# Kernel tuning notes

Hardware: AMD Instinct MI355X
Metric: run time of the kernel (lower is better)

## Reference

```python
import jax, jax.numpy as jnp
import numpy as np

# ---- static config ----
B, D, H, W, C = 4, 8, 56, 56, 192
Md, Mh, Mw = 2, 7, 7
Sd, Sh, Sw = 1, 3, 3
NH = 6
HD = C // NH
SCALE = HD ** -0.5
N = Md * Mh * Mw  # 98
NW = (D // Md) * (H // Mh) * (W // Mw)  # 256 windows per batch element


def _rel_pos_index():
    coords = np.stack(np.meshgrid(np.arange(Md), np.arange(Mh), np.arange(Mw), indexing='ij'))
    cf = coords.reshape(3, -1)
    rc = (cf[:, :, None] - cf[:, None, :]).transpose(1, 2, 0)
    rc[..., 0] += Md - 1
    rc[..., 1] += Mh - 1
    rc[..., 2] += Mw - 1
    rc[..., 0] *= (2 * Mh - 1) * (2 * Mw - 1)
    rc[..., 1] *= 2 * Mw - 1
    return rc.sum(-1)  # (N, N) int

REL_IDX = jnp.asarray(_rel_pos_index())


def _build_attn_mask():
    img = np.zeros((D, H, W), dtype=np.float32)
    cnt = 0
    for ds in (slice(0, -Md), slice(-Md, -Sd), slice(-Sd, None)):
        for hs in (slice(0, -Mh), slice(-Mh, -Sh), slice(-Sh, None)):
            for ws in (slice(0, -Mw), slice(-Mw, -Sw), slice(-Sw, None)):
                img[ds, hs, ws] = cnt
                cnt += 1
    mw = img.reshape(D // Md, Md, H // Mh, Mh, W // Mw, Mw)
    mw = mw.transpose(0, 2, 4, 1, 3, 5).reshape(-1, N)  # (NW, N)
    am = mw[:, None, :] - mw[:, :, None]
    return np.where(am != 0, -100.0, 0.0).astype(np.float32)  # (NW, N, N)


def window_partition(x):  # (B, D, H, W, C) -> (B*NW, N, C)
    x = x.reshape(B, D // Md, Md, H // Mh, Mh, W // Mw, Mw, C)
    return x.transpose(0, 1, 3, 5, 2, 4, 6, 7).reshape(-1, N, C)


def window_reverse(w):  # (B*NW, N, C) -> (B, D, H, W, C)
    x = w.reshape(B, D // Md, H // Mh, W // Mw, Md, Mh, Mw, C)
    return x.transpose(0, 1, 4, 2, 5, 3, 6, 7).reshape(B, D, H, W, C)


def layer_norm(x, g, b, eps=1e-5):
    mu = x.mean(-1, keepdims=True)
    var = ((x - mu) ** 2).mean(-1, keepdims=True)
    return (x - mu) * jax.lax.rsqrt(var + eps) * g + b


def setup_inputs() -> dict:
    key = jax.random.key(0)
    ks = jax.random.split(key, 6)
    return {
        'x': jax.random.normal(ks[0], (B, D * H * W, C), jnp.float32),
        'attn_mask': jnp.asarray(_build_attn_mask()),
        'norm1_g': jnp.ones((C,), jnp.float32),
        'norm1_b': jnp.zeros((C,), jnp.float32),
        'qkv_w': jax.random.normal(ks[1], (3 * C, C), jnp.float32) * 0.02,
        'qkv_b': jnp.zeros((3 * C,), jnp.float32),
        'rel_bias': jax.random.normal(ks[2], ((2 * Md - 1) * (2 * Mh - 1) * (2 * Mw - 1), NH), jnp.float32) * 0.02,
        'proj_w': jax.random.normal(ks[3], (C, C), jnp.float32) * 0.02,
        'proj_b': jnp.zeros((C,), jnp.float32),
        'fc1_w': jax.random.normal(ks[4], (C, C), jnp.float32) * 0.02,
        'fc1_b': jnp.zeros((C,), jnp.float32),
    }


def reference(x, attn_mask, norm1_g, norm1_b, qkv_w, qkv_b, rel_bias, proj_w, proj_b, fc1_w, fc1_b):
    shortcut = x
    h = layer_norm(x, norm1_g, norm1_b).reshape(B, D, H, W, C)
    # cyclic shift (dims divisible by window -> no padding needed)
    h = jnp.roll(h, shift=(-Sd, -Sh, -Sw), axis=(1, 2, 3))
    xw = window_partition(h)  # (B*NW, N, C)
    B_ = xw.shape[0]
    qkv = (xw @ qkv_w.T + qkv_b).reshape(B_, N, 3, NH, HD).transpose(2, 0, 3, 1, 4)
    q, k, v = qkv[0], qkv[1], qkv[2]  # (B_, NH, N, HD)
    attn = jnp.einsum('bhnd,bhmd->bhnm', q * SCALE, k)
    bias = rel_bias[REL_IDX.reshape(-1)].reshape(N, N, NH).transpose(2, 0, 1)  # (NH, N, N)
    attn = attn + bias[None]
    # additive shift mask per window
    attn = attn.reshape(B, NW, NH, N, N) + attn_mask[None, :, None]
    attn = jax.nn.softmax(attn.reshape(B_, NH, N, N), axis=-1)
    out = jnp.einsum('bhnm,bhmd->bhnd', attn, v).transpose(0, 2, 1, 3).reshape(B_, N, C)
    out = out @ proj_w.T + proj_b
    h = window_reverse(out)
    h = jnp.roll(h, shift=(Sd, Sh, Sw), axis=(1, 2, 3)).reshape(B, D * H * W, C)
    h = jax.nn.gelu(h @ fc1_w.T + fc1_b, approximate=False)
    return shortcut + h
```

## Files before the change

kernel.cpp:

```cpp
#include <hip/hip_runtime.h>
#include <cstdint>
#include <cstddef>

typedef __bf16 bf16_t;
typedef __bf16 bf16x8 __attribute__((ext_vector_type(8)));
typedef float  f32x4  __attribute__((ext_vector_type(4)));

#define DHW   25088
#define SCALE 0.17677669529663687f

__device__ inline f32x4 mfma16(bf16x8 a, bf16x8 b, f32x4 c) {
  return __builtin_amdgcn_mfma_f32_16x16x32_bf16(a, b, c, 0, 0, 0);
}

__device__ inline size_t wrow_to_grow(int orow) {
  int win = orow / 98, tok = orow % 98;
  int b = win >> 8, wr = win & 255;
  int bd = wr >> 6, bh = (wr >> 3) & 7, bwi = wr & 7;
  int md = tok / 49, mh = (tok / 7) % 7, mw = tok % 7;
  int d = (bd * 2 + md + 1) & 7;
  int h = bh * 7 + mh + 3; if (h >= 56) h -= 56;
  int w = bwi * 7 + mw + 3; if (w >= 56) w -= 56;
  return (size_t)b * DHW + (size_t)((d * 56 + h) * 56 + w);
}

__global__ __launch_bounds__(256) void prep_kernel(
    const float* __restrict__ qkv_w, const float* __restrict__ proj_w,
    const float* __restrict__ fc1_w,
    bf16_t* __restrict__ wq, bf16_t* __restrict__ wp, bf16_t* __restrict__ wf)
{
  int idx = blockIdx.x * 256 + threadIdx.x;
  if (idx < 110592) { wq[idx] = (bf16_t)qkv_w[idx]; return; }
  idx -= 110592;
  if (idx < 36864) { wp[idx] = (bf16_t)proj_w[idx]; return; }
  idx -= 36864;
  if (idx < 36864) { wf[idx] = (bf16_t)fc1_w[idx]; }
}

__global__ __launch_bounds__(256) void prep_bm_kernel(
    const float* __restrict__ rel_bias, const float* __restrict__ mask,
    bf16_t* __restrict__ bmr)
{
  int idx = blockIdx.x * 256 + threadIdx.x;
  int e    = idx & 31;
  int lane = (idx >> 5) & 63;
  int t2   = idx >> 11;
  int mt   = t2 % 7;
  int wh   = t2 / 7;
  int type = wh / 6, h = wh - type * 6;
  int winb = ((type & 4) ? 3 : 0) * 64 + ((type & 2) ? 7 : 0) * 8 + ((type & 1) ? 7 : 0);
  int g = lane >> 4, li = lane & 15;
  int nt2 = e >> 2, v = e & 3;
  int row = mt * 16 + g * 4 + v;
  int col = nt2 * 16 + li;
  float val = -1e30f;
  if (row < 98 && col < 98 && nt2 < 7) {
    int di = row / 49 - col / 49 + 1;
    int hi = (row / 7) % 7 - (col / 7) % 7 + 6;
    int wi = row % 7 - col % 7 + 6;
    int rid = di * 169 + hi * 13 + wi;
    val = mask[winb * 9604 + row * 98 + col] + rel_bias[rid * 6 + h];
  }
  bmr[idx] = (bf16_t)val;
}

__global__ __launch_bounds__(256, 3) void lnqkv_kernel(
    const float* __restrict__ x, const float* __restrict__ gw,
    const float* __restrict__ bw_, const bf16_t* __restrict__ wq,
    const float* __restrict__ qkv_b, bf16_t* __restrict__ qkv)
{
  __shared__ __align__(16) bf16_t As[64][200];
  __shared__ __align__(16) bf16_t Bs[64][200];
  __shared__ float gws[192], bws[192], bias[576];
  int tid = threadIdx.x;
  int row0 = blockIdx.x * 64;
  if (tid < 192) { gws[tid] = gw[tid]; bws[tid] = bw_[tid]; }
  for (int c = tid; c < 576; c += 256) bias[c] = qkv_b[c];

  {
    int r = tid >> 2, part = tid & 3;
    size_t grow = wrow_to_grow(row0 + r);
    const float* xr = x + grow * 192 + part * 48;
    float v[48];
    #pragma unroll
    for (int i = 0; i < 12; i++) *(float4*)&v[i * 4] = *(const float4*)(xr + i * 4);
    float s = 0.f, sq = 0.f;
    #pragma unroll
    for (int i = 0; i < 48; i++) { s += v[i]; sq += v[i] * v[i]; }
    s += __shfl_xor(s, 1, 64); sq += __shfl_xor(sq, 1, 64);
    s += __shfl_xor(s, 2, 64); sq += __shfl_xor(sq, 2, 64);
    float mu = s * (1.0f / 192.0f);
    float var = sq * (1.0f / 192.0f) - mu * mu;
    float rstd = rsqrtf(var + 1e-5f);
    __syncthreads();
    bf16_t nb[48];
    #pragma unroll
    for (int i = 0; i < 48; i++) {
      int c = part * 48 + i;
      nb[i] = (bf16_t)((v[i] - mu) * rstd * gws[c] + bws[c]);
    }
    #pragma unroll
    for (int j = 0; j < 6; j++)
      *(bf16x8*)&As[r][part * 48 + j * 8] = *(bf16x8*)&nb[j * 8];
  }
  __syncthreads();

  int wid = tid >> 6, lane = tid & 63;
  int wm = wid >> 1, wn = wid & 1;
  int g = lane >> 4, li = lane & 15;
  bf16x8 afr[2][6];
  #pragma unroll
  for (int ks = 0; ks < 6; ks++) {
    afr[0][ks] = *(const bf16x8*)&As[wm * 32 + li][ks * 32 + g * 8];
    afr[1][ks] = *(const bf16x8*)&As[wm * 32 + 16 + li][ks * 32 + g * 8];
  }

  uint4 st[6];
  #pragma unroll
  for (int i = 0; i < 6; i++) {
    int c = tid + 256 * i; int rr = c / 24, ck = c % 24;
    st[i] = *(const uint4*)(wq + (size_t)rr * 192 + ck * 8);
  }
  for (int nt = 0; nt < 9; nt++) {
    __syncthreads();
    #pragma unroll
    for (int i = 0; i < 6; i++) {
      int c = tid + 256 * i; int rr = c / 24, ck = c % 24;
      *(uint4*)&Bs[rr][ck * 8] = st[i];
    }
    __syncthreads();
    if (nt < 8) {
      #pragma unroll
      for (int i = 0; i < 6; i++) {
        int c = tid + 256 * i; int rr = c / 24, ck = c % 24;
        st[i] = *(const uint4*)(wq + (size_t)(nt + 1) * 12288 + (size_t)rr * 192 + ck * 8);
      }
    }
    f32x4 acc[2][2] = {};
    #pragma unroll
    for (int ks = 0; ks < 6; ks++) {
      int ko = ks * 32 + g * 8;
      bf16x8 b0 = *(const bf16x8*)&Bs[wn * 32 + li][ko];
      bf16x8 b1 = *(const bf16x8*)&Bs[wn * 32 + 16 + li][ko];
      acc[0][0] = mfma16(afr[0][ks], b0, acc[0][0]);
      acc[0][1] = mfma16(afr[0][ks], b1, acc[0][1]);
      acc[1][0] = mfma16(afr[1][ks], b0, acc[1][0]);
      acc[1][1] = mfma16(afr[1][ks], b1, acc[1][1]);
    }
    #pragma unroll
    for (int mi = 0; mi < 2; mi++)
    #pragma unroll
    for (int ni = 0; ni < 2; ni++)
    #pragma unroll
    for (int v = 0; v < 4; v++) {
      int row = row0 + wm * 32 + mi * 16 + g * 4 + v;
      int col = nt * 64 + wn * 32 + ni * 16 + li;
      qkv[(size_t)row * 576 + col] = (bf16_t)(acc[mi][ni][v] + bias[col]);
    }
  }
}

__global__ __launch_bounds__(448, 6) void attn_kernel(
    const bf16_t* __restrict__ qkv, const bf16_t* __restrict__ bmr,
    bf16_t* __restrict__ ao)
{
  __shared__ __align__(16) bf16_t U[15232];
  __shared__ __align__(16) bf16_t Vt[32][136];
  int bid = blockIdx.x;
  int h = bid % 6, win = bid / 6;
  int winb = win & 255;
  int type = (((winb >> 6) == 3) ? 4 : 0) | ((((winb >> 3) & 7) == 7) ? 2 : 0)
           | (((winb & 7) == 7) ? 1 : 0);
  int tid = threadIdx.x;
  int wid = tid >> 6, lane = tid & 63;
  int mt = wid, g = lane >> 4, li = lane & 15;

  const bf16_t* bmp = bmr + ((((size_t)(type * 6 + h)) * 7 + mt) * 64 + lane) * 32;
  bf16x8 bm0 = *(const bf16x8*)(bmp);
  bf16x8 bm1 = *(const bf16x8*)(bmp + 8);
  bf16x8 bm2 = *(const bf16x8*)(bmp + 16);
  bf16x8 bm3 = *(const bf16x8*)(bmp + 24);

  const bf16_t* base = qkv + (size_t)win * 98 * 576 + h * 32;
  #define QS(r, c) U[(r) * 40 + (c)]
  #define KS(r, c) U[4480 + (r) * 40 + (c)]
  #define PS(r, c) U[(r) * 136 + (c)]
  for (int c = tid; c < 784; c += 448) {
    int cc = c < 392 ? c : c - 392;
    int tok = cc >> 2, part = cc & 3;
    uint4 u = *(const uint4*)(base + (c < 392 ? 0 : 192) + tok * 576 + part * 8);
    if (c < 392) *(uint4*)&QS(tok, part * 8) = u;
    else         *(uint4*)&KS(tok, part * 8) = u;
  }
  if (tid < 112) {
    uint4 z = {0, 0, 0, 0};
    int a = tid >> 6;
    int r = 98 + ((tid & 63) >> 2), part = tid & 3;
    if (r < 112) {
      if (a == 0) *(uint4*)&QS(r, part * 8) = z;
      else        *(uint4*)&KS(r, part * 8) = z;
    }
  }
  if (tid < 392) {
    int tok = tid >> 2, part = tid & 3;
    bf16x8 u = *(const bf16x8*)(base + 384 + tok * 576 + part * 8);
    #pragma unroll
    for (int j = 0; j < 8; j++) Vt[part * 8 + j][tok] = u[j];
  }
  for (int e2 = tid; e2 < 960; e2 += 448) {
    int r = e2 / 30, ci = 98 + e2 % 30;
    Vt[r][ci] = (bf16_t)0.0f;
  }
  __syncthreads();

  bf16x8 af = *(const bf16x8*)&QS(mt * 16 + li, g * 8);
  float logit[7][4];
  #pragma unroll
  for (int nt2 = 0; nt2 < 7; nt2++) {
    bf16x8 bfr = *(const bf16x8*)&KS(nt2 * 16 + li, g * 8);
    f32x4 z = {};
    f32x4 S = mfma16(af, bfr, z);
    #pragma unroll
    for (int v = 0; v < 4; v++) {
      int e = nt2 * 4 + v;
      float bmv = (e < 8) ? (float)bm0[e] : (e < 16) ? (float)bm1[e - 8]
                : (e < 24) ? (float)bm2[e - 16] : (float)bm3[e - 24];
      logit[nt2][v] = S[v] * SCALE + bmv;
    }
  }
  __syncthreads();

  #pragma unroll
  for (int v = 0; v < 4; v++) {
    float mx = logit[0][v];
    #pragma unroll
    for (int nt2 = 1; nt2 < 7; nt2++) mx = fmaxf(mx, logit[nt2][v]);
    #pragma unroll
    for (int off = 1; off < 16; off <<= 1) mx = fmaxf(mx, __shfl_xor(mx, off, 64));
    float se = 0.f;
    #pragma unroll
    for (int nt2 = 0; nt2 < 7; nt2++) {
      float p = __expf(logit[nt2][v] - mx);
      logit[nt2][v] = p; se += p;
    }
    #pragma unroll
    for (int off = 1; off < 16; off <<= 1) se += __shfl_xor(se, off, 64);
    float inv = 1.0f / se;
    int row = mt * 16 + g * 4 + v;
    #pragma unroll
    for (int nt2 = 0; nt2 < 7; nt2++)
      PS(row, nt2 * 16 + li) = (bf16_t)(logit[nt2][v] * inv);
    PS(row, 112 + li) = (bf16_t)0.0f;
  }
  f32x4 o0 = {}, o1 = {};
  #pragma unroll
  for (int ks = 0; ks < 4; ks++) {
    int ko = ks * 32 + g * 8;
    bf16x8 pf = *(const bf16x8*)&PS(mt * 16 + li, ko);
    bf16x8 v0 = *(const bf16x8*)&Vt[li][ko];
    bf16x8 v1 = *(const bf16x8*)&Vt[16 + li][ko];
    o0 = mfma16(pf, v0, o0);
    o1 = mfma16(pf, v1, o1);
  }
  bf16_t* aout = ao + (size_t)win * 98 * 192 + h * 32;
  #pragma unroll
  for (int v = 0; v < 4; v++) {
    int row = mt * 16 + g * 4 + v;
    if (row < 98) {
      aout[(size_t)row * 192 + li]      = (bf16_t)o0[v];
      aout[(size_t)row * 192 + 16 + li] = (bf16_t)o1[v];
    }
  }
  #undef QS
  #undef KS
  #undef PS
}

__global__ __launch_bounds__(256, 3) void pf_kernel(
    const bf16_t* __restrict__ ao, const bf16_t* __restrict__ wp,
    const float* __restrict__ proj_b, const bf16_t* __restrict__ wf,
    const float* __restrict__ fc1_b, const float* __restrict__ x,
    float* __restrict__ out)
{
  __shared__ __align__(16) bf16_t As[64][200];
  __shared__ __align__(16) bf16_t Bs[64][200];
  __shared__ float pb[192], fb[192];
  int tid = threadIdx.x;
  int row0 = blockIdx.x * 64;
  if (tid < 192) { pb[tid] = proj_b[tid]; fb[tid] = fc1_b[tid]; }
  #pragma unroll
  for (int i = 0; i < 6; i++) {
    int c = tid + 256 * i; int rr = c / 24, ck = c % 24;
    *(uint4*)&As[rr][ck * 8] = *(const uint4*)(ao + (size_t)(row0 + rr) * 192 + ck * 8);
  }
  __syncthreads();

  int wid = tid >> 6, lane = tid & 63;
  int wm = wid >> 1, wn = wid & 1;
  int g = lane >> 4, li = lane & 15;
  bf16x8 afr[2][6];
  #pragma unroll
  for (int ks = 0; ks < 6; ks++) {
    afr[0][ks] = *(const bf16x8*)&As[wm * 32 + li][ks * 32 + g * 8];
    afr[1][ks] = *(const bf16x8*)&As[wm * 32 + 16 + li][ks * 32 + g * 8];
  }
  __syncthreads();

  uint4 st[6];
  #pragma unroll
  for (int i = 0; i < 6; i++) {
    int c = tid + 256 * i; int rr = c / 24, ck = c % 24;
    st[i] = *(const uint4*)(wp + (size_t)rr * 192 + ck * 8);
  }
  for (int nt = 0; nt < 3; nt++) {
    __syncthreads();
    #pragma unroll
    for (int i = 0; i < 6; i++) {
      int c = tid + 256 * i; int rr = c / 24, ck = c % 24;
      *(uint4*)&Bs[rr][ck * 8] = st[i];
    }
    __syncthreads();
    if (nt < 2) {
      #pragma unroll
      for (int i = 0; i < 6; i++) {
        int c = tid + 256 * i; int rr = c / 24, ck = c % 24;
        st[i] = *(const uint4*)(wp + (size_t)(nt + 1) * 12288 + (size_t)rr * 192 + ck * 8);
      }
    }
    f32x4 acc[2][2] = {};
    #pragma unroll
    for (int ks = 0; ks < 6; ks++) {
      int ko = ks * 32 + g * 8;
      bf16x8 b0 = *(const bf16x8*)&Bs[wn * 32 + li][ko];
      bf16x8 b1 = *(const bf16x8*)&Bs[wn * 32 + 16 + li][ko];
      acc[0][0] = mfma16(afr[0][ks], b0, acc[0][0]);
      acc[0][1] = mfma16(afr[0][ks], b1, acc[0][1]);
      acc[1][0] = mfma16(afr[1][ks], b0, acc[1][0]);
      acc[1][1] = mfma16(afr[1][ks], b1, acc[1][1]);
    }
    #pragma unroll
    for (int mi = 0; mi < 2; mi++)
    #pragma unroll
    for (int ni = 0; ni < 2; ni++)
    #pragma unroll
    for (int v = 0; v < 4; v++) {
      int rloc = wm * 32 + mi * 16 + g * 4 + v;
      int col = nt * 64 + wn * 32 + ni * 16 + li;
      As[rloc][col] = (bf16_t)(acc[mi][ni][v] + pb[col]);
    }
  }
  __syncthreads();

  bf16x8 a2[2][6];
  #pragma unroll
  for (int ks = 0; ks < 6; ks++) {
    a2[0][ks] = *(const bf16x8*)&As[wm * 32 + li][ks * 32 + g * 8];
    a2[1][ks] = *(const bf16x8*)&As[wm * 32 + 16 + li][ks * 32 + g * 8];
  }
  #pragma unroll
  for (int i = 0; i < 6; i++) {
    int c = tid + 256 * i; int rr = c / 24, ck = c % 24;
    st[i] = *(const uint4*)(wf + (size_t)rr * 192 + ck * 8);
  }
  for (int nt = 0; nt < 3; nt++) {
    __syncthreads();
    #pragma unroll
    for (int i = 0; i < 6; i++) {
      int c = tid + 256 * i; int rr = c / 24, ck = c % 24;
      *(uint4*)&Bs[rr][ck * 8] = st[i];
    }
    __syncthreads();
    if (nt < 2) {
      #pragma unroll
      for (int i = 0; i < 6; i++) {
        int c = tid + 256 * i; int rr = c / 24, ck = c % 24;
        st[i] = *(const uint4*)(wf + (size_t)(nt + 1) * 12288 + (size_t)rr * 192 + ck * 8);
      }
    }
    f32x4 acc[2][2] = {};
    #pragma unroll
    for (int ks = 0; ks < 6; ks++) {
      int ko = ks * 32 + g * 8;
      bf16x8 b0 = *(const bf16x8*)&Bs[wn * 32 + li][ko];
      bf16x8 b1 = *(const bf16x8*)&Bs[wn * 32 + 16 + li][ko];
      acc[0][0] = mfma16(a2[0][ks], b0, acc[0][0]);
      acc[0][1] = mfma16(a2[0][ks], b1, acc[0][1]);
      acc[1][0] = mfma16(a2[1][ks], b0, acc[1][0]);
      acc[1][1] = mfma16(a2[1][ks], b1, acc[1][1]);
    }
    #pragma unroll
    for (int mi = 0; mi < 2; mi++)
    #pragma unroll
    for (int v = 0; v < 4; v++) {
      int rloc = wm * 32 + mi * 16 + g * 4 + v;
      size_t grow = wrow_to_grow(row0 + rloc);
      #pragma unroll
      for (int ni = 0; ni < 2; ni++) {
        int col = nt * 64 + wn * 32 + ni * 16 + li;
        float val = acc[mi][ni][v] + fb[col];
        float ge = 0.5f * val * (1.0f + erff(val * 0.70710678118654752f));
        size_t o = grow * 192 + col;
        out[o] = x[o] + ge;
      }
    }
  }
}

extern "C" void kernel_launch(void* const* d_in, const int* in_sizes, int n_in,
                              void* d_out, int out_size, void* d_ws, size_t ws_size,
                              hipStream_t stream) {
  (void)in_sizes; (void)n_in; (void)out_size; (void)ws_size;
  const float* x         = (const float*)d_in[0];
  const float* attn_mask = (const float*)d_in[1];
  const float* n1g       = (const float*)d_in[2];
  const float* n1b       = (const float*)d_in[3];
  const float* qkv_w     = (const float*)d_in[4];
  const float* qkv_b     = (const float*)d_in[5];
  const float* rel_bias  = (const float*)d_in[6];
  const float* proj_w    = (const float*)d_in[7];
  const float* proj_b    = (const float*)d_in[8];
  const float* fc1_w     = (const float*)d_in[9];
  const float* fc1_b     = (const float*)d_in[10];
  float* out = (float*)d_out;

  char* ws = (char*)d_ws;
  size_t off = 0;
  auto alloc = [&](size_t bytes) -> char* {
    char* p = ws + off;
    off += (bytes + 255) & ~(size_t)255;
    return p;
  };
  bf16_t* wq  = (bf16_t*)alloc(110592 * 2);
  bf16_t* wp  = (bf16_t*)alloc(36864 * 2);
  bf16_t* wf  = (bf16_t*)alloc(36864 * 2);
  bf16_t* bmr = (bf16_t*)alloc((size_t)688128 * 2);
  bf16_t* qkv = (bf16_t*)alloc((size_t)100352 * 576 * 2);
  bf16_t* ao  = (bf16_t*)alloc((size_t)100352 * 192 * 2);

  prep_kernel<<<720, 256, 0, stream>>>(qkv_w, proj_w, fc1_w, wq, wp, wf);
  prep_bm_kernel<<<2688, 256, 0, stream>>>(rel_bias, attn_mask, bmr);
  lnqkv_kernel<<<1568, 256, 0, stream>>>(x, n1g, n1b, wq, qkv_b, qkv);
  attn_kernel<<<6144, 448, 0, stream>>>(qkv, bmr, ao);
  pf_kernel<<<1568, 256, 0, stream>>>(ao, wp, proj_b, wf, fc1_b, x, out);
}
```

Before: 430.9 us.

## Fuse LN+QKV, windowed attention, proj and FC1 into one per-window kernel

Replaces the three kernels (LN+QKV GEMM, per-head attention, proj+FC1) with one kernel that handles a whole 98-token window per block across all six heads. Q, K, V and the attention output stay in LDS, so the large bf16 qkv and ao intermediates are never written to or read back from global memory. Q is pre-scaled before being stored. The cost is a 163 KB LDS footprint, which allows only one 7-wave block per CU, plus a serial loop over heads with many barriers. This lower occupancy may limit latency hiding.

```diff
diff --git a/kernel.cpp b/kernel.cpp
--- a/kernel.cpp
+++ b/kernel.cpp
@@ -64,346 +64,334 @@
   bmr[idx] = (bf16_t)val;
 }
 
-__global__ __launch_bounds__(256, 3) void lnqkv_kernel(
+__global__ __launch_bounds__(448, 2) void fused_kernel(
     const float* __restrict__ x, const float* __restrict__ gw,
     const float* __restrict__ bw_, const bf16_t* __restrict__ wq,
-    const float* __restrict__ qkv_b, bf16_t* __restrict__ qkv)
+    const float* __restrict__ qkv_b, const bf16_t* __restrict__ wp,
+    const float* __restrict__ proj_b, const bf16_t* __restrict__ wf,
+    const float* __restrict__ fc1_b, const bf16_t* __restrict__ bmr,
+    float* __restrict__ out)
 {
-  __shared__ __align__(16) bf16_t As[64][200];
-  __shared__ __align__(16) bf16_t Bs[64][200];
-  __shared__ float gws[192], bws[192], bias[576];
-  int tid = threadIdx.x;
-  int row0 = blockIdx.x * 64;
-  if (tid < 192) { gws[tid] = gw[tid]; bws[tid] = bw_[tid]; }
-  for (int c = tid; c < 576; c += 256) bias[c] = qkv_b[c];
-
-  {
-    int r = tid >> 2, part = tid & 3;
-    size_t grow = wrow_to_grow(row0 + r);
-    const float* xr = x + grow * 192 + part * 48;
-    float v[48];
-    #pragma unroll
-    for (int i = 0; i < 12; i++) *(float4*)&v[i * 4] = *(const float4*)(xr + i * 4);
-    float s = 0.f, sq = 0.f;
-    #pragma unroll
-    for (int i = 0; i < 48; i++) { s += v[i]; sq += v[i] * v[i]; }
-    s += __shfl_xor(s, 1, 64); sq += __shfl_xor(sq, 1, 64);
-    s += __shfl_xor(s, 2, 64); sq += __shfl_xor(sq, 2, 64);
-    float mu = s * (1.0f / 192.0f);
-    float var = sq * (1.0f / 192.0f) - mu * mu;
-    float rstd = rsqrtf(var + 1e-5f);
-    __syncthreads();
-    bf16_t nb[48];
-    #pragma unroll
-    for (int i = 0; i < 48; i++) {
-      int c = part * 48 + i;
-      nb[i] = (bf16_t)((v[i] - mu) * rstd * gws[c] + bws[c]);
-    }
-    #pragma unroll
-    for (int j = 0; j < 6; j++)
-      *(bf16x8*)&As[r][part * 48 + j * 8] = *(bf16x8*)&nb[j * 8];
-  }
-  __syncthreads();
-
-  int wid = tid >> 6, lane = tid & 63;
-  int wm = wid >> 1, wn = wid & 1;
-  int g = lane >> 4, li = lane & 15;
-  bf16x8 afr[2][6];
-  #pragma unroll
-  for (int ks = 0; ks < 6; ks++) {
-    afr[0][ks] = *(const bf16x8*)&As[wm * 32 + li][ks * 32 + g * 8];
-    afr[1][ks] = *(const bf16x8*)&As[wm * 32 + 16 + li][ks * 32 + g * 8];
-  }
-
-  uint4 st[6];
-  #pragma unroll
-  for (int i = 0; i < 6; i++) {
-    int c = tid + 256 * i; int rr = c / 24, ck = c % 24;
-    st[i] = *(const uint4*)(wq + (size_t)rr * 192 + ck * 8);
-  }
-  for (int nt = 0; nt < 9; nt++) {
-    __syncthreads();
-    #pragma unroll
-    for (int i = 0; i < 6; i++) {
-      int c = tid + 256 * i; int rr = c / 24, ck = c % 24;
-      *(uint4*)&Bs[rr][ck * 8] = st[i];
-    }
-    __syncthreads();
-    if (nt < 8) {
-      #pragma unroll
-      for (int i = 0; i < 6; i++) {
-        int c = tid + 256 * i; int rr = c / 24, ck = c % 24;
-        st[i] = *(const uint4*)(wq + (size_t)(nt + 1) * 12288 + (size_t)rr * 192 + ck * 8);
-      }
-    }
-    f32x4 acc[2][2] = {};
-    #pragma unroll
-    for (int ks = 0; ks < 6; ks++) {
-      int ko = ks * 32 + g * 8;
-      bf16x8 b0 = *(const bf16x8*)&Bs[wn * 32 + li][ko];
-      bf16x8 b1 = *(const bf16x8*)&Bs[wn * 32 + 16 + li][ko];
-      acc[0][0] = mfma16(afr[0][ks], b0, acc[0][0]);
-      acc[0][1] = mfma16(afr[0][ks], b1, acc[0][1]);
-      acc[1][0] = mfma16(afr[1][ks], b0, acc[1][0]);
-      acc[1][1] = mfma16(afr[1][ks], b1, acc[1][1]);
-    }
-    #pragma unroll
-    for (int mi = 0; mi < 2; mi++)
-    #pragma unroll
-    for (int ni = 0; ni < 2; ni++)
-    #pragma unroll
-    for (int v = 0; v < 4; v++) {
-      int row = row0 + wm * 32 + mi * 16 + g * 4 + v;
-      int col = nt * 64 + wn * 32 + ni * 16 + li;
-      qkv[(size_t)row * 576 + col] = (bf16_t)(acc[mi][ni][v] + bias[col]);
-    }
-  }
-}
-
-__global__ __launch_bounds__(448, 6) void attn_kernel(
-    const bf16_t* __restrict__ qkv, const bf16_t* __restrict__ bmr,
-    bf16_t* __restrict__ ao)
-{
-  __shared__ __align__(16) bf16_t U[15232];
-  __shared__ __align__(16) bf16_t Vt[32][136];
-  int bid = blockIdx.x;
-  int h = bid % 6, win = bid / 6;
+  __shared__ __align__(16) char smem[163392];
+  bf16_t* U  = (bf16_t*)smem;
+  bf16_t* Qs = (bf16_t*)(smem + 30464);
+  bf16_t* Ks = (bf16_t*)(smem + 69664);
+  bf16_t* Vt = (bf16_t*)(smem + 108864);
+  float*  qb = (float*)(smem + 161088);
+  float* gwb = (float*)smem;
+
+  #define BS(r, c)  U[(r) * 200 + (c)]
+  #define PSd(r, c) U[(r) * 136 + (c)]
+  #define QS(r, c)  Qs[(r) * 200 + (c)]
+  #define KS(r, c)  Ks[(r) * 200 + (c)]
+  #define VT(d, t)  Vt[(d) * 136 + (t)]
+
+  int win  = blockIdx.x;
   int winb = win & 255;
   int type = (((winb >> 6) == 3) ? 4 : 0) | ((((winb >> 3) & 7) == 7) ? 2 : 0)
            | (((winb & 7) == 7) ? 1 : 0);
-  int tid = threadIdx.x;
-  int wid = tid >> 6, lane = tid & 63;
-  int mt = wid, g = lane >> 4, li = lane & 15;
-
-  const bf16_t* bmp = bmr + ((((size_t)(type * 6 + h)) * 7 + mt) * 64 + lane) * 32;
-  bf16x8 bm0 = *(const bf16x8*)(bmp);
-  bf16x8 bm1 = *(const bf16x8*)(bmp + 8);
-  bf16x8 bm2 = *(const bf16x8*)(bmp + 16);
-  bf16x8 bm3 = *(const bf16x8*)(bmp + 24);
-
-  const bf16_t* base = qkv + (size_t)win * 98 * 576 + h * 32;
-  #define QS(r, c) U[(r) * 40 + (c)]
-  #define KS(r, c) U[4480 + (r) * 40 + (c)]
-  #define PS(r, c) U[(r) * 136 + (c)]
-  for (int c = tid; c < 784; c += 448) {
-    int cc = c < 392 ? c : c - 392;
-    int tok = cc >> 2, part = cc & 3;
-    uint4 u = *(const uint4*)(base + (c < 392 ? 0 : 192) + tok * 576 + part * 8);
-    if (c < 392) *(uint4*)&QS(tok, part * 8) = u;
-    else         *(uint4*)&KS(tok, part * 8) = u;
-  }
-  if (tid < 112) {
-    uint4 z = {0, 0, 0, 0};
-    int a = tid >> 6;
-    int r = 98 + ((tid & 63) >> 2), part = tid & 3;
-    if (r < 112) {
-      if (a == 0) *(uint4*)&QS(r, part * 8) = z;
-      else        *(uint4*)&KS(r, part * 8) = z;
-    }
-  }
-  if (tid < 392) {
-    int tok = tid >> 2, part = tid & 3;
-    bf16x8 u = *(const bf16x8*)(base + 384 + tok * 576 + part * 8);
-    #pragma unroll
-    for (int j = 0; j < 8; j++) Vt[part * 8 + j][tok] = u[j];
-  }
-  for (int e2 = tid; e2 < 960; e2 += 448) {
-    int r = e2 / 30, ci = 98 + e2 % 30;
-    Vt[r][ci] = (bf16_t)0.0f;
-  }
+  int tid  = threadIdx.x;
+  int wid  = tid >> 6, lane = tid & 63;
+  int g = lane >> 4, li = lane & 15;
+
+  if (tid < 192) { gwb[tid] = gw[tid]; gwb[192 + tid] = bw_[tid]; }
+  for (int c = tid; c < 576; c += 448) qb[c] = qkv_b[c];
+  {
+    uint4 z = {0u, 0u, 0u, 0u};
+    for (int c = tid; c < 768; c += 448) {
+      int d = c >> 2, part = c & 3;
+      *(uint4*)&VT(d, 96 + part * 8) = z;
+    }
+  }
+
+  int r = wid * 16 + li;
+  float v[48];
+  if (r < 98) {
+    size_t growr = wrow_to_grow(win * 98 + r);
+    const float* xr = x + growr * 192 + g * 8;
+    #pragma unroll
+    for (int ks = 0; ks < 6; ks++) {
+      *(float4*)&v[ks * 8]     = *(const float4*)(xr + ks * 32);
+      *(float4*)&v[ks * 8 + 4] = *(const float4*)(xr + ks * 32 + 4);
+    }
+  } else {
+    #pragma unroll
+    for (int i = 0; i < 48; i++) v[i] = 0.f;
+  }
+  float s = 0.f, sq = 0.f;
+  #pragma unroll
+  for (int i = 0; i < 48; i++) { s += v[i]; sq += v[i] * v[i]; }
+  s += __shfl_xor(s, 16, 64); sq += __shfl_xor(sq, 16, 64);
+  s += __shfl_xor(s, 32, 64); sq += __shfl_xor(sq, 32, 64);
+  float mu   = s * (1.0f / 192.0f);
+  float var  = sq * (1.0f / 192.0f) - mu * mu;
+  float rstd = rsqrtf(var + 1e-5f);
   __syncthreads();
-
-  bf16x8 af = *(const bf16x8*)&QS(mt * 16 + li, g * 8);
-  float logit[7][4];
-  #pragma unroll
-  for (int nt2 = 0; nt2 < 7; nt2++) {
-    bf16x8 bfr = *(const bf16x8*)&KS(nt2 * 16 + li, g * 8);
-    f32x4 z = {};
-    f32x4 S = mfma16(af, bfr, z);
-    #pragma unroll
-    for (int v = 0; v < 4; v++) {
-      int e = nt2 * 4 + v;
-      float bmv = (e < 8) ? (float)bm0[e] : (e < 16) ? (float)bm1[e - 8]
-                : (e < 24) ? (float)bm2[e - 16] : (float)bm3[e - 24];
-      logit[nt2][v] = S[v] * SCALE + bmv;
+  bf16x8 afr[6];
+  #pragma unroll
+  for (int ks = 0; ks < 6; ks++) {
+    bf16x8 t;
+    #pragma unroll
+    for (int j = 0; j < 8; j++) {
+      int c = ks * 32 + g * 8 + j;
+      t[j] = (r < 98) ? (bf16_t)((v[ks * 8 + j] - mu) * rstd * gwb[c] + gwb[192 + c])
+                      : (bf16_t)0.0f;
+    }
+    afr[ks] = t;
+  }
+
+  uint4 st[4];
+  #pragma unroll
+  for (int i = 0; i < 4; i++) {
+    int c = tid + 448 * i;
+    if (i < 3 || c < 1536) {
+      int rr = c / 24, ck = c % 24;
+      st[i] = *(const uint4*)(wq + (size_t)rr * 192 + ck * 8);
+    }
+  }
+  for (int nt = 0; nt < 9; nt++) {
+    __syncthreads();
+    #pragma unroll
+    for (int i = 0; i < 4; i++) {
+      int c = tid + 448 * i;
+      if (i < 3 || c < 1536) {
+        int rr = c / 24, ck = c % 24;
+        *(uint4*)&BS(rr, ck * 8) = st[i];
+      }
+    }
+    __syncthreads();
+    if (nt < 8) {
+      #pragma unroll
+      for (int i = 0; i < 4; i++) {
+        int c = tid + 448 * i;
+        if (i < 3 || c < 1536) {
+          int rr = c / 24, ck = c % 24;
+          st[i] = *(const uint4*)(wq + (size_t)(nt + 1) * 12288 + (size_t)rr * 192 + ck * 8);
+        }
+      }
+    }
+    f32x4 acc[4] = {};
+    #pragma unroll
+    for (int ks = 0; ks < 6; ks++) {
+      bf16x8 a = afr[ks];
+      #pragma unroll
+      for (int ni = 0; ni < 4; ni++) {
+        bf16x8 b = *(const bf16x8*)&BS(ni * 16 + li, ks * 32 + g * 8);
+        acc[ni] = mfma16(a, b, acc[ni]);
+      }
+    }
+    #pragma unroll
+    for (int ni = 0; ni < 4; ni++)
+    #pragma unroll
+    for (int vv = 0; vv < 4; vv++) {
+      int row = wid * 16 + g * 4 + vv;
+      if (row < 98) {
+        int col = nt * 64 + ni * 16 + li;
+        float val = acc[ni][vv] + qb[col];
+        if (nt < 3)      QS(row, col)       = (bf16_t)(val * SCALE);
+        else if (nt < 6) KS(row, col - 192) = (bf16_t)val;
+        else             VT(col - 384, row) = (bf16_t)val;
+      }
     }
   }
   __syncthreads();
 
-  #pragma unroll
-  for (int v = 0; v < 4; v++) {
-    float mx = logit[0][v];
-    #pragma unroll
-    for (int nt2 = 1; nt2 < 7; nt2++) mx = fmaxf(mx, logit[nt2][v]);
-    #pragma unroll
-    for (int off = 1; off < 16; off <<= 1) mx = fmaxf(mx, __shfl_xor(mx, off, 64));
-    float se = 0.f;
+  int mt  = wid;
+  int rq  = mt * 16 + li;
+  int rqc = rq < 98 ? rq : 97;
+  for (int h = 0; h < 6; h++) {
+    const bf16_t* bmp = bmr + ((((size_t)(type * 6 + h)) * 7 + mt) * 64 + lane) * 32;
+    bf16x8 bm0 = *(const bf16x8*)(bmp);
+    bf16x8 bm1 = *(const bf16x8*)(bmp + 8);
+    bf16x8 bm2 = *(const bf16x8*)(bmp + 16);
+    bf16x8 bm3 = *(const bf16x8*)(bmp + 24);
+    bf16x8 af = *(const bf16x8*)&QS(rqc, h * 32 + g * 8);
+    float logit[7][4];
     #pragma unroll
     for (int nt2 = 0; nt2 < 7; nt2++) {
-      float p = __expf(logit[nt2][v] - mx);
-      logit[nt2][v] = p; se += p;
-    }
-    #pragma unroll
-    for (int off = 1; off < 16; off <<= 1) se += __shfl_xor(se, off, 64);
-    float inv = 1.0f / se;
-    int row = mt * 16 + g * 4 + v;
-    #pragma unroll
-    for (int nt2 = 0; nt2 < 7; nt2++)
-      PS(row, nt2 * 16 + li) = (bf16_t)(logit[nt2][v] * inv);
-    PS(row, 112 + li) = (bf16_t)0.0f;
-  }
-  f32x4 o0 = {}, o1 = {};
-  #pragma unroll
-  for (int ks = 0; ks < 4; ks++) {
-    int ko = ks * 32 + g * 8;
-    bf16x8 pf = *(const bf16x8*)&PS(mt * 16 + li, ko);
-    bf16x8 v0 = *(const bf16x8*)&Vt[li][ko];
-    bf16x8 v1 = *(const bf16x8*)&Vt[16 + li][ko];
-    o0 = mfma16(pf, v0, o0);
-    o1 = mfma16(pf, v1, o1);
-  }
-  bf16_t* aout = ao + (size_t)win * 98 * 192 + h * 32;
-  #pragma unroll
-  for (int v = 0; v < 4; v++) {
-    int row = mt * 16 + g * 4 + v;
-    if (row < 98) {
-      aout[(size_t)row * 192 + li]      = (bf16_t)o0[v];
-      aout[(size_t)row * 192 + 16 + li] = (bf16_t)o1[v];
-    }
-  }
+      int rk = nt2 * 16 + li;
+      int rkc = rk < 98 ? rk : 97;
+      bf16x8 bfr = *(const bf16x8*)&KS(rkc, h * 32 + g * 8);
+      f32x4 z = {};
+      f32x4 S = mfma16(af, bfr, z);
+      #pragma unroll
+      for (int vv = 0; vv < 4; vv++) {
+        int e = nt2 * 4 + vv;
+        float bmv = (e < 8) ? (float)bm0[e] : (e < 16) ? (float)bm1[e - 8]
+                  : (e < 24) ? (float)bm2[e - 16] : (float)bm3[e - 24];
+        logit[nt2][vv] = S[vv] + bmv;
+      }
+    }
+    #pragma unroll
+    for (int vv = 0; vv < 4; vv++) {
+      float mx = logit[0][vv];
+      #pragma unroll
+      for (int nt2 = 1; nt2 < 7; nt2++) mx = fmaxf(mx, logit[nt2][vv]);
+      #pragma unroll
+      for (int off = 1; off < 16; off <<= 1) mx = fmaxf(mx, __shfl_xor(mx, off, 64));
+      float se = 0.f;
+      #pragma unroll
+      for (int nt2 = 0; nt2 < 7; nt2++) {
+        float p = __expf(logit[nt2][vv] - mx);
+        logit[nt2][vv] = p; se += p;
+      }
+      #pragma unroll
+      for (int off = 1; off < 16; off <<= 1) se += __shfl_xor(se, off, 64);
+      float inv = 1.0f / se;
+      int row = mt * 16 + g * 4 + vv;
+      #pragma unroll
+      for (int nt2 = 0; nt2 < 7; nt2++)
+        PSd(row, nt2 * 16 + li) = (bf16_t)(logit[nt2][vv] * inv);
+      PSd(row, 112 + li) = (bf16_t)0.0f;
+    }
+    f32x4 o0 = {}, o1 = {};
+    #pragma unroll
+    for (int ks = 0; ks < 4; ks++) {
+      int ko = ks * 32 + g * 8;
+      bf16x8 pf = *(const bf16x8*)&PSd(mt * 16 + li, ko);
+      bf16x8 v0 = *(const bf16x8*)&VT(h * 32 + li, ko);
+      bf16x8 v1 = *(const bf16x8*)&VT(h * 32 + 16 + li, ko);
+      o0 = mfma16(pf, v0, o0);
+      o1 = mfma16(pf, v1, o1);
+    }
+    #pragma unroll
+    for (int vv = 0; vv < 4; vv++) {
+      int row = mt * 16 + g * 4 + vv;
+      if (row < 98) {
+        QS(row, h * 32 + li)      = (bf16_t)o0[vv];
+        QS(row, h * 32 + 16 + li) = (bf16_t)o1[vv];
+      }
+    }
+  }
+
+  float* bfb = qb;
+  if (tid < 192) bfb[tid] = proj_b[tid];
+  bf16x8 a2[6];
+  #pragma unroll
+  for (int ks = 0; ks < 6; ks++)
+    a2[ks] = *(const bf16x8*)&QS(rqc, ks * 32 + g * 8);
+  #pragma unroll
+  for (int i = 0; i < 4; i++) {
+    int c = tid + 448 * i;
+    if (i < 3 || c < 1536) {
+      int rr = c / 24, ck = c % 24;
+      st[i] = *(const uint4*)(wp + (size_t)rr * 192 + ck * 8);
+    }
+  }
+  for (int nt = 0; nt < 3; nt++) {
+    __syncthreads();
+    #pragma unroll
+    for (int i = 0; i < 4; i++) {
+      int c = tid + 448 * i;
+      if (i < 3 || c < 1536) {
+        int rr = c / 24, ck = c % 24;
+        *(uint4*)&BS(rr, ck * 8) = st[i];
+      }
+    }
+    __syncthreads();
+    if (nt < 2) {
+      #pragma unroll
+      for (int i = 0; i < 4; i++) {
+        int c = tid + 448 * i;
+        if (i < 3 || c < 1536) {
+          int rr = c / 24, ck = c % 24;
+          st[i] = *(const uint4*)(wp + (size_t)(nt + 1) * 12288 + (size_t)rr * 192 + ck * 8);
+        }
+      }
+    }
+    f32x4 acc[4] = {};
+    #pragma unroll
+    for (int ks = 0; ks < 6; ks++) {
+      bf16x8 a = a2[ks];
+      #pragma unroll
+      for (int ni = 0; ni < 4; ni++) {
+        bf16x8 b = *(const bf16x8*)&BS(ni * 16 + li, ks * 32 + g * 8);
+        acc[ni] = mfma16(a, b, acc[ni]);
+      }
+    }
+    #pragma unroll
+    for (int ni = 0; ni < 4; ni++)
+    #pragma unroll
+    for (int vv = 0; vv < 4; vv++) {
+      int row = wid * 16 + g * 4 + vv;
+      if (row < 98) {
+        int col = nt * 64 + ni * 16 + li;
+        KS(row, col) = (bf16_t)(acc[ni][vv] + bfb[col]);
+      }
+    }
+  }
+
+  bf16x8 a3[6];
+  #pragma unroll
+  for (int ks = 0; ks < 6; ks++)
+    a3[ks] = *(const bf16x8*)&KS(rqc, ks * 32 + g * 8);
+  #pragma unroll
+  for (int i = 0; i < 4; i++) {
+    int c = tid + 448 * i;
+    if (i < 3 || c < 1536) {
+      int rr = c / 24, ck = c % 24;
+      st[i] = *(const uint4*)(wf + (size_t)rr * 192 + ck * 8);
+    }
+  }
+  size_t growv[4];
+  #pragma unroll
+  for (int vv = 0; vv < 4; vv++) {
+    int row = wid * 16 + g * 4 + vv;
+    growv[vv] = (row < 98) ? wrow_to_grow(win * 98 + row) : (size_t)0;
+  }
+  for (int nt = 0; nt < 3; nt++) {
+    __syncthreads();
+    #pragma unroll
+    for (int i = 0; i < 4; i++) {
+      int c = tid + 448 * i;
+      if (i < 3 || c < 1536) {
+        int rr = c / 24, ck = c % 24;
+        *(uint4*)&BS(rr, ck * 8) = st[i];
+      }
+    }
+    if (nt == 0 && tid < 192) bfb[tid] = fc1_b[tid];
+    __syncthreads();
+    if (nt < 2) {
+      #pragma unroll
+      for (int i = 0; i < 4; i++) {
+        int c = tid + 448 * i;
+        if (i < 3 || c < 1536) {
+          int rr = c / 24, ck = c % 24;
+          st[i] = *(const uint4*)(wf + (size_t)(nt + 1) * 12288 + (size_t)rr * 192 + ck * 8);
+        }
+      }
+    }
+    f32x4 acc[4] = {};
+    #pragma unroll
+    for (int ks = 0; ks < 6; ks++) {
+      bf16x8 a = a3[ks];
+      #pragma unroll
+      for (int ni = 0; ni < 4; ni++) {
+        bf16x8 b = *(const bf16x8*)&BS(ni * 16 + li, ks * 32 + g * 8);
+        acc[ni] = mfma16(a, b, acc[ni]);
+      }
+    }
+    #pragma unroll
+    for (int vv = 0; vv < 4; vv++) {
+      int row = wid * 16 + g * 4 + vv;
+      if (row < 98) {
+        const float* xr = x + growv[vv] * 192;
+        float* op = out + growv[vv] * 192;
+        #pragma unroll
+        for (int ni = 0; ni < 4; ni++) {
+          int col = nt * 64 + ni * 16 + li;
+          float val = acc[ni][vv] + bfb[col];
+          float ge = 0.5f * val * (1.0f + erff(val * 0.70710678118654752f));
+          op[col] = xr[col] + ge;
+        }
+      }
+    }
+  }
+  #undef BS
+  #undef PSd
   #undef QS
   #undef KS
-  #undef PS
-}
-
-__global__ __launch_bounds__(256, 3) void pf_kernel(
-    const bf16_t* __restrict__ ao, const bf16_t* __restrict__ wp,
-    const float* __restrict__ proj_b, const bf16_t* __restrict__ wf,
-    const float* __restrict__ fc1_b, const float* __restrict__ x,
-    float* __restrict__ out)
-{
-  __shared__ __align__(16) bf16_t As[64][200];
-  __shared__ __align__(16) bf16_t Bs[64][200];
-  __shared__ float pb[192], fb[192];
-  int tid = threadIdx.x;
-  int row0 = blockIdx.x * 64;
-  if (tid < 192) { pb[tid] = proj_b[tid]; fb[tid] = fc1_b[tid]; }
-  #pragma unroll
-  for (int i = 0; i < 6; i++) {
-    int c = tid + 256 * i; int rr = c / 24, ck = c % 24;
-    *(uint4*)&As[rr][ck * 8] = *(const uint4*)(ao + (size_t)(row0 + rr) * 192 + ck * 8);
-  }
-  __syncthreads();
-
-  int wid = tid >> 6, lane = tid & 63;
-  int wm = wid >> 1, wn = wid & 1;
-  int g = lane >> 4, li = lane & 15;
-  bf16x8 afr[2][6];
-  #pragma unroll
-  for (int ks = 0; ks < 6; ks++) {
-    afr[0][ks] = *(const bf16x8*)&As[wm * 32 + li][ks * 32 + g * 8];
-    afr[1][ks] = *(const bf16x8*)&As[wm * 32 + 16 + li][ks * 32 + g * 8];
-  }
-  __syncthreads();
-
-  uint4 st[6];
-  #pragma unroll
-  for (int i = 0; i < 6; i++) {
-    int c = tid + 256 * i; int rr = c / 24, ck = c % 24;
-    st[i] = *(const uint4*)(wp + (size_t)rr * 192 + ck * 8);
-  }
-  for (int nt = 0; nt < 3; nt++) {
-    __syncthreads();
-    #pragma unroll
-    for (int i = 0; i < 6; i++) {
-      int c = tid + 256 * i; int rr = c / 24, ck = c % 24;
-      *(uint4*)&Bs[rr][ck * 8] = st[i];
-    }
-    __syncthreads();
-    if (nt < 2) {
-      #pragma unroll
-      for (int i = 0; i < 6; i++) {
-        int c = tid + 256 * i; int rr = c / 24, ck = c % 24;
-        st[i] = *(const uint4*)(wp + (size_t)(nt + 1) * 12288 + (size_t)rr * 192 + ck * 8);
-      }
-    }
-    f32x4 acc[2][2] = {};
-    #pragma unroll
-    for (int ks = 0; ks < 6; ks++) {
-      int ko = ks * 32 + g * 8;
-      bf16x8 b0 = *(const bf16x8*)&Bs[wn * 32 + li][ko];
-      bf16x8 b1 = *(const bf16x8*)&Bs[wn * 32 + 16 + li][ko];
-      acc[0][0] = mfma16(afr[0][ks], b0, acc[0][0]);
-      acc[0][1] = mfma16(afr[0][ks], b1, acc[0][1]);
-      acc[1][0] = mfma16(afr[1][ks], b0, acc[1][0]);
-      acc[1][1] = mfma16(afr[1][ks], b1, acc[1][1]);
-    }
-    #pragma unroll
-    for (int mi = 0; mi < 2; mi++)
-    #pragma unroll
-    for (int ni = 0; ni < 2; ni++)
-    #pragma unroll
-    for (int v = 0; v < 4; v++) {
-      int rloc = wm * 32 + mi * 16 + g * 4 + v;
-      int col = nt * 64 + wn * 32 + ni * 16 + li;
-      As[rloc][col] = (bf16_t)(acc[mi][ni][v] + pb[col]);
-    }
-  }
-  __syncthreads();
-
-  bf16x8 a2[2][6];
-  #pragma unroll
-  for (int ks = 0; ks < 6; ks++) {
-    a2[0][ks] = *(const bf16x8*)&As[wm * 32 + li][ks * 32 + g * 8];
-    a2[1][ks] = *(const bf16x8*)&As[wm * 32 + 16 + li][ks * 32 + g * 8];
-  }
-  #pragma unroll
-  for (int i = 0; i < 6; i++) {
-    int c = tid + 256 * i; int rr = c / 24, ck = c % 24;
-    st[i] = *(const uint4*)(wf + (size_t)rr * 192 + ck * 8);
-  }
-  for (int nt = 0; nt < 3; nt++) {
-    __syncthreads();
-    #pragma unroll
-    for (int i = 0; i < 6; i++) {
-      int c = tid + 256 * i; int rr = c / 24, ck = c % 24;
-      *(uint4*)&Bs[rr][ck * 8] = st[i];
-    }
-    __syncthreads();
-    if (nt < 2) {
-      #pragma unroll
-      for (int i = 0; i < 6; i++) {
-        int c = tid + 256 * i; int rr = c / 24, ck = c % 24;
-        st[i] = *(const uint4*)(wf + (size_t)(nt + 1) * 12288 + (size_t)rr * 192 + ck * 8);
-      }
-    }
-    f32x4 acc[2][2] = {};
-    #pragma unroll
-    for (int ks = 0; ks < 6; ks++) {
-      int ko = ks * 32 + g * 8;
-      bf16x8 b0 = *(const bf16x8*)&Bs[wn * 32 + li][ko];
-      bf16x8 b1 = *(const bf16x8*)&Bs[wn * 32 + 16 + li][ko];
-      acc[0][0] = mfma16(a2[0][ks], b0, acc[0][0]);
-      acc[0][1] = mfma16(a2[0][ks], b1, acc[0][1]);
-      acc[1][0] = mfma16(a2[1][ks], b0, acc[1][0]);
-      acc[1][1] = mfma16(a2[1][ks], b1, acc[1][1]);
-    }
-    #pragma unroll
-    for (int mi = 0; mi < 2; mi++)
-    #pragma unroll
-    for (int v = 0; v < 4; v++) {
-      int rloc = wm * 32 + mi * 16 + g * 4 + v;
-      size_t grow = wrow_to_grow(row0 + rloc);
-      #pragma unroll
-      for (int ni = 0; ni < 2; ni++) {
-        int col = nt * 64 + wn * 32 + ni * 16 + li;
-        float val = acc[mi][ni][v] + fb[col];
-        float ge = 0.5f * val * (1.0f + erff(val * 0.70710678118654752f));
-        size_t o = grow * 192 + col;
-        out[o] = x[o] + ge;
-      }
-    }
-  }
+  #undef VT
 }
 
 extern "C" void kernel_launch(void* const* d_in, const int* in_sizes, int n_in,
@@ -434,12 +422,9 @@
   bf16_t* wp  = (bf16_t*)alloc(36864 * 2);
   bf16_t* wf  = (bf16_t*)alloc(36864 * 2);
   bf16_t* bmr = (bf16_t*)alloc((size_t)688128 * 2);
-  bf16_t* qkv = (bf16_t*)alloc((size_t)100352 * 576 * 2);
-  bf16_t* ao  = (bf16_t*)alloc((size_t)100352 * 192 * 2);
 
   prep_kernel<<<720, 256, 0, stream>>>(qkv_w, proj_w, fc1_w, wq, wp, wf);
   prep_bm_kernel<<<2688, 256, 0, stream>>>(rel_bias, attn_mask, bmr);
-  lnqkv_kernel<<<1568, 256, 0, stream>>>(x, n1g, n1b, wq, qkv_b, qkv);
-  attn_kernel<<<6144, 448, 0, stream>>>(qkv, bmr, ao);
-  pf_kernel<<<1568, 256, 0, stream>>>(ao, wp, proj_b, wf, fc1_b, x, out);
-}
+  fused_kernel<<<1024, 448, 0, stream>>>(x, n1g, n1b, wq, qkv_b, wp, proj_b,
+                                         wf, fc1_b, bmr, out);
+}
```

Result: no change. 433.2 us (+0.6%).
